# Kernel tuning notes

Measured on AMD Instinct MI355X. Metric: run time of the kernel, lower is better.

The kernel has to match this reference:

```python
import jax, jax.numpy as jnp
import numpy as np

B, LI, LC = 2, 1024, 256
H, NH, HD = 1024, 16, 64
MLP = 4096
EPS = 1e-6


def rmsnorm(x, w):
    return x * jax.lax.rsqrt(jnp.mean(x * x, axis=-1, keepdims=True) + EPS) * w


def apply_rope(x, cos, sin):
    # x: [B, NH, S, HD]; cos/sin: [S, HD]; rotate-half convention
    x1, x2 = jnp.split(x, 2, axis=-1)
    rot = jnp.concatenate([-x2, x1], axis=-1)
    return x * cos + rot * sin


def project_qkv(x, w, b):
    # x: [B, S, H] -> q,k,v each [B, NH, S, HD]
    bsz, s, _ = x.shape
    qkv = (x @ w.T + b).reshape(bsz, s, 3, NH, HD)
    qkv = jnp.transpose(qkv, (2, 0, 3, 1, 4))
    return qkv[0], qkv[1], qkv[2]


def setup_inputs() -> dict:
    key = jax.random.key(0)
    ks = iter(jax.random.split(key, 40))
    n = lambda shape, scale=1.0: jax.random.normal(next(ks), shape, dtype=jnp.float32) * scale
    xav = lambda fo, fi: n((fo, fi), float(np.sqrt(2.0 / (fo + fi))))
    inp = {
        'image_tokens': n((B, LI, H)),
        'condition_tokens': n((B, LC, H)),
        'image_rope_cos': n((LI, HD)),
        'image_rope_sin': n((LI, HD)),
        'cond_rope_cos': n((LC, HD)),
        'cond_rope_sin': n((LC, HD)),
        'img_norm1_w': jnp.ones((H,)), 'cond_norm1_w': jnp.ones((H,)),
        'img_qkv_w': xav(3 * H, H), 'img_qkv_b': jnp.zeros((3 * H,)),
        'cond_qkv_w': xav(3 * H, H), 'cond_qkv_b': jnp.zeros((3 * H,)),
        'img_qn_w': jnp.ones((HD,)), 'img_kn_w': jnp.ones((HD,)),
        'cond_qn_w': jnp.ones((HD,)), 'cond_kn_w': jnp.ones((HD,)),
        'img_out_w': xav(H, H), 'img_out_b': jnp.zeros((H,)),
        'cond_out_w': xav(H, H), 'cond_out_b': jnp.zeros((H,)),
        'img_norm2_w': jnp.ones((H,)), 'cond_norm2_w': jnp.ones((H,)),
        'img_mlp_w1': xav(MLP, H), 'img_mlp_b1': jnp.zeros((MLP,)),
        'img_mlp_w2': xav(MLP, H), 'img_mlp_b2': jnp.zeros((MLP,)),
        'img_mlp_w3': xav(H, MLP), 'img_mlp_b3': jnp.zeros((H,)),
        'cond_mlp_w1': xav(MLP, H), 'cond_mlp_b1': jnp.zeros((MLP,)),
        'cond_mlp_w2': xav(MLP, H), 'cond_mlp_b2': jnp.zeros((MLP,)),
        'cond_mlp_w3': xav(H, MLP), 'cond_mlp_b3': jnp.zeros((H,)),
        'alpha': jnp.zeros((1,)), 'beta': jnp.zeros((1,)),
    }
    return inp


def swiglu(x, w1, b1, w2, b2, w3, b3):
    return (jax.nn.silu(x @ w1.T + b1) * (x @ w2.T + b2)) @ w3.T + b3


def reference(image_tokens, condition_tokens, image_rope_cos, image_rope_sin,
              cond_rope_cos, cond_rope_sin, img_norm1_w, cond_norm1_w,
              img_qkv_w, img_qkv_b, cond_qkv_w, cond_qkv_b,
              img_qn_w, img_kn_w, cond_qn_w, cond_kn_w,
              img_out_w, img_out_b, cond_out_w, cond_out_b,
              img_norm2_w, cond_norm2_w,
              img_mlp_w1, img_mlp_b1, img_mlp_w2, img_mlp_b2, img_mlp_w3, img_mlp_b3,
              cond_mlp_w1, cond_mlp_b1, cond_mlp_w2, cond_mlp_b2, cond_mlp_w3, cond_mlp_b3,
              alpha, beta):
    img_res, cond_res = image_tokens, condition_tokens
    iq, ik, iv = project_qkv(rmsnorm(image_tokens, img_norm1_w), img_qkv_w, img_qkv_b)
    cq, ck, cv = project_qkv(rmsnorm(condition_tokens, cond_norm1_w), cond_qkv_w, cond_qkv_b)
    iq = apply_rope(rmsnorm(iq, img_qn_w), image_rope_cos, image_rope_sin)
    ik = apply_rope(rmsnorm(ik, img_kn_w), image_rope_cos, image_rope_sin)
    cq = apply_rope(rmsnorm(cq, cond_qn_w), cond_rope_cos, cond_rope_sin)
    ck = apply_rope(rmsnorm(ck, cond_kn_w), cond_rope_cos, cond_rope_sin)
    q = jnp.concatenate([cq, iq], axis=2)  # [B, NH, LC+LI, HD]
    k = jnp.concatenate([ck, ik], axis=2)
    v = jnp.concatenate([cv, iv], axis=2)
    scores = jnp.einsum('bhqd,bhkd->bhqk', q, k) / jnp.sqrt(jnp.float32(HD)).astype(q.dtype)
    attn = jax.nn.softmax(scores, axis=-1)
    out = jnp.einsum('bhqk,bhkd->bhqd', attn, v)
    cond_o, img_o = out[:, :, :LC], out[:, :, LC:]
    cond_o = jnp.transpose(cond_o, (0, 2, 1, 3)).reshape(B, LC, H)
    img_o = jnp.transpose(img_o, (0, 2, 1, 3)).reshape(B, LI, H)
    condition_tokens = cond_res + (cond_o @ cond_out_w.T + cond_out_b)
    image_tokens = img_res + alpha.reshape(1, 1, 1) * (img_o @ img_out_w.T + img_out_b)
    condition_tokens = condition_tokens + swiglu(rmsnorm(condition_tokens, cond_norm2_w),
                                                 cond_mlp_w1, cond_mlp_b1, cond_mlp_w2, cond_mlp_b2, cond_mlp_w3, cond_mlp_b3)
    image_tokens = image_tokens + beta.reshape(1, 1, 1) * swiglu(rmsnorm(image_tokens, img_norm2_w),
                                                                 img_mlp_w1, img_mlp_b1, img_mlp_w2, img_mlp_b2, img_mlp_w3, img_mlp_b3)
    return image_tokens, condition_tokens
```

## Files before the change

### kernel.cpp

```cpp
#include <hip/hip_runtime.h>
#include <hip/hip_bf16.h>

#define BB   2
#define LI   1024
#define LC   256
#define SEQ  1280
#define HDIM 1024
#define NH   16
#define HD   64
#define MLPD 4096
#define EPS  1e-6f
#define MROWS 2560
#define MTI  16
#define MTT  20

typedef __bf16 bf16x8 __attribute__((ext_vector_type(8)));
typedef float f32x4 __attribute__((ext_vector_type(4)));
typedef unsigned short us4 __attribute__((ext_vector_type(4)));
typedef unsigned short us8 __attribute__((ext_vector_type(8)));

static __device__ __forceinline__ unsigned short f2bf(float f) {
    unsigned int u = __builtin_bit_cast(unsigned int, f);
    u += 0x7fffu + ((u >> 16) & 1u);
    return (unsigned short)(u >> 16);
}
static __device__ __forceinline__ float bf2f(unsigned short h) {
    unsigned int u = ((unsigned int)h) << 16;
    return __builtin_bit_cast(float, u);
}

static __device__ __forceinline__ void gload_lds16(const void* g, void* l) {
    __builtin_amdgcn_global_load_lds((__attribute__((address_space(1))) void*)(g),
                                     (__attribute__((address_space(3))) void*)(l),
                                     16, 0, 0);
}

__global__ __launch_bounds__(256)
void pack_weights(const float* __restrict__ w1i, const float* __restrict__ w2i,
                  const float* __restrict__ w1c, const float* __restrict__ w2c,
                  const float* __restrict__ w3i, const float* __restrict__ w3c,
                  const float* __restrict__ wqi, const float* __restrict__ wqc,
                  const float* __restrict__ woi, const float* __restrict__ woc,
                  unsigned short* __restrict__ wpi, unsigned short* __restrict__ wpc,
                  unsigned short* __restrict__ w3bi, unsigned short* __restrict__ w3bc,
                  unsigned short* __restrict__ wqbi, unsigned short* __restrict__ wqbc,
                  unsigned short* __restrict__ wobi, unsigned short* __restrict__ wobc)
{
    const int seg = blockIdx.y;
    const float* s0 = nullptr; const float* s1 = nullptr;
    unsigned short* dst = nullptr; int n4 = 0; bool pair = false;
    switch (seg) {
        case 0: pair = true; s0 = w1i; s1 = w2i; dst = wpi;  n4 = 8388608 / 4; break;
        case 1: pair = true; s0 = w1c; s1 = w2c; dst = wpc;  n4 = 8388608 / 4; break;
        case 2: s0 = w3i; dst = w3bi; n4 = 4194304 / 4; break;
        case 3: s0 = w3c; dst = w3bc; n4 = 4194304 / 4; break;
        case 4: s0 = wqi; dst = wqbi; n4 = 3145728 / 4; break;
        case 5: s0 = wqc; dst = wqbc; n4 = 3145728 / 4; break;
        case 6: s0 = woi; dst = wobi; n4 = 1048576 / 4; break;
        case 7: s0 = woc; dst = wobc; n4 = 1048576 / 4; break;
    }
    for (int i = blockIdx.x * 256 + threadIdx.x; i < n4; i += gridDim.x * 256) {
        float4 v;
        if (pair) {
            int p  = i >> 8;
            int k4 = i & 255;
            int g = p >> 4, r = p & 15;
            const float* s = (g & 1) ? s1 : s0;
            v = *(const float4*)&s[((size_t)((g >> 1) * 16 + r)) * 1024 + k4 * 4];
        } else {
            v = ((const float4*)s0)[i];
        }
        us4 o = { f2bf(v.x), f2bf(v.y), f2bf(v.z), f2bf(v.w) };
        ((us4*)dst)[i] = o;
    }
}

__global__ __launch_bounds__(256)
void rmsnorm1(const float* __restrict__ img, const float* __restrict__ cond,
              const float* __restrict__ wi, const float* __restrict__ wc,
              unsigned short* __restrict__ xn)
{
    const int row = blockIdx.x;
    const int t   = threadIdx.x;
    const float* x = (row < 2048) ? img + (size_t)row * HDIM
                                  : cond + (size_t)(row - 2048) * HDIM;
    const float* w = (row < 2048) ? wi : wc;
    float4 v = ((const float4*)x)[t];
    float ss = v.x*v.x + v.y*v.y + v.z*v.z + v.w*v.w;
    for (int o = 32; o > 0; o >>= 1) ss += __shfl_xor(ss, o);
    __shared__ float red[4];
    if ((t & 63) == 0) red[t >> 6] = ss;
    __syncthreads();
    float inv = rsqrtf((red[0]+red[1]+red[2]+red[3]) * (1.0f / HDIM) + EPS);
    float4 wv = ((const float4*)w)[t];
    us4 pk = { f2bf(v.x*inv*wv.x), f2bf(v.y*inv*wv.y),
               f2bf(v.z*inv*wv.z), f2bf(v.w*inv*wv.w) };
    *(us4*)&xn[(size_t)row * HDIM + t * 4] = pk;
}

__global__ __launch_bounds__(256)
void rmsnorm2(const float* __restrict__ img_tok, const float* __restrict__ cond_tok,
              const float* __restrict__ op, const float* __restrict__ wi,
              const float* __restrict__ wc, const float* __restrict__ alpha,
              unsigned short* __restrict__ n2)
{
    const int row = blockIdx.x;
    const int t   = threadIdx.x;
    const bool img = row < 2048;
    const float sc = img ? alpha[0] : 1.0f;
    const float* tok = img ? img_tok + (size_t)row * HDIM
                           : cond_tok + (size_t)(row - 2048) * HDIM;
    const float* w = img ? wi : wc;
    float4 tv = ((const float4*)tok)[t];
    float4 ov = ((const float4*)(op + (size_t)row * HDIM))[t];
    float4 v = { tv.x + sc*ov.x, tv.y + sc*ov.y, tv.z + sc*ov.z, tv.w + sc*ov.w };
    float ss = v.x*v.x + v.y*v.y + v.z*v.z + v.w*v.w;
    for (int o = 32; o > 0; o >>= 1) ss += __shfl_xor(ss, o);
    __shared__ float red[4];
    if ((t & 63) == 0) red[t >> 6] = ss;
    __syncthreads();
    float inv = rsqrtf((red[0]+red[1]+red[2]+red[3]) * (1.0f / HDIM) + EPS);
    float4 wv = ((const float4*)w)[t];
    us4 pk = { f2bf(v.x*inv*wv.x), f2bf(v.y*inv*wv.y),
               f2bf(v.z*inv*wv.z), f2bf(v.w*inv*wv.w) };
    *(us4*)&n2[(size_t)row * HDIM + t * 4] = pk;
}

__global__ __launch_bounds__(256)
void op_init(const float* __restrict__ bi, const float* __restrict__ bc,
             float* __restrict__ op)
{
    const int row = blockIdx.x, t = threadIdx.x;
    const float* b = (row < 2048) ? bi : bc;
    ((float4*)(op + (size_t)row * HDIM))[t] = ((const float4*)b)[t];
}

__global__ __launch_bounds__(256)
void down_init(const float* __restrict__ img_tok, const float* __restrict__ cond_tok,
               const float* __restrict__ op, const float* __restrict__ b3i,
               const float* __restrict__ b3c, const float* __restrict__ alpha,
               const float* __restrict__ beta, float* __restrict__ out)
{
    const int row = blockIdx.x, t = threadIdx.x;
    const bool img = row < 2048;
    const float sa = img ? alpha[0] : 1.0f;
    const float sm = img ? beta[0]  : 1.0f;
    const float* tok = img ? img_tok + (size_t)row * HDIM
                           : cond_tok + (size_t)(row - 2048) * HDIM;
    const float* b3 = img ? b3i : b3c;
    float4 tv = ((const float4*)tok)[t];
    float4 ov = ((const float4*)(op + (size_t)row * HDIM))[t];
    float4 bv = ((const float4*)b3)[t];
    float4 o4 = { tv.x + sa*ov.x + sm*bv.x, tv.y + sa*ov.y + sm*bv.y,
                  tv.z + sa*ov.z + sm*bv.z, tv.w + sa*ov.w + sm*bv.w };
    ((float4*)(out + (size_t)row * HDIM))[t] = o4;
}

__global__ __launch_bounds__(256)
void qkv_gemm(const unsigned short* __restrict__ xn,
              const unsigned short* __restrict__ wqi, const unsigned short* __restrict__ wqc,
              const float* __restrict__ bi, const float* __restrict__ bc,
              unsigned short* __restrict__ qh, unsigned short* __restrict__ kh,
              unsigned short* __restrict__ vt)
{
    __shared__ __align__(16) unsigned short As[128][32];
    __shared__ __align__(16) unsigned short Ws[128][32];

    const int mt = blockIdx.x;
    const bool img = mt < MTI;
    const int row0 = img ? mt * 128 : 2048 + (mt - MTI) * 128;
    const int grow0 = img ? mt * 128 : (mt - MTI) * 128;
    const unsigned short* W = img ? wqi : wqc;
    const float* bias = img ? bi : bc;
    const int bn = blockIdx.y * 128;

    const int t = threadIdx.x, lane = t & 63, wid = t >> 6;
    const int wm = wid >> 1, wn = wid & 1;
    const int srow = (wid << 5) + (lane >> 2);
    const int scol = (lane & 3) << 3;
    const unsigned short* Ag0 = xn + (size_t)(row0 + srow)      * HDIM + scol;
    const unsigned short* Ag1 = xn + (size_t)(row0 + srow + 16) * HDIM + scol;
    const unsigned short* Wg0 = W  + (size_t)(bn + srow)        * HDIM + scol;
    const unsigned short* Wg1 = W  + (size_t)(bn + srow + 16)   * HDIM + scol;
    unsigned short* lA0 = &As[(wid << 5)     ][0];
    unsigned short* lA1 = &As[(wid << 5) + 16][0];
    unsigned short* lW0 = &Ws[(wid << 5)     ][0];
    unsigned short* lW1 = &Ws[(wid << 5) + 16][0];

    const int fr = lane & 15, kg = lane >> 4, ko = kg << 3;
    f32x4 acc[4][4] = {};

    for (int k0 = 0; k0 < HDIM; k0 += 32) {
        __syncthreads();
        gload_lds16(Ag0 + k0, lA0);
        gload_lds16(Ag1 + k0, lA1);
        gload_lds16(Wg0 + k0, lW0);
        gload_lds16(Wg1 + k0, lW1);
        __syncthreads();
        bf16x8 aF[4], bF[4];
#pragma unroll
        for (int m = 0; m < 4; ++m) aF[m] = *(const bf16x8*)&As[wm*64 + m*16 + fr][ko];
#pragma unroll
        for (int n = 0; n < 4; ++n) bF[n] = *(const bf16x8*)&Ws[wn*64 + n*16 + fr][ko];
#pragma unroll
        for (int m = 0; m < 4; ++m)
#pragma unroll
            for (int n = 0; n < 4; ++n)
                acc[m][n] = __builtin_amdgcn_mfma_f32_16x16x32_bf16(aF[m], bF[n], acc[m][n], 0,0,0);
    }

#pragma unroll
    for (int n = 0; n < 4; ++n) {
        const int gc = bn + wn*64 + n*16 + fr;
        const int which = gc >> 10;
        const int h = (gc >> 6) & 15, d = gc & 63;
        const float bv = bias[gc];
#pragma unroll
        for (int m = 0; m < 4; ++m) {
            const int gl0 = grow0 + wm*64 + m*16 + (kg << 2);
            int b, s0;
            if (img) { b = gl0 >> 10; s0 = LC + (gl0 & 1023); }
            else     { b = gl0 >> 8;  s0 = gl0 & 255; }
            if (which == 2) {
                us4 pk = { f2bf(acc[m][n][0] + bv), f2bf(acc[m][n][1] + bv),
                           f2bf(acc[m][n][2] + bv), f2bf(acc[m][n][3] + bv) };
                *(us4*)&vt[(((size_t)(b*NH + h)) * HD + d) * SEQ + s0] = pk;
            } else {
                unsigned short* dst = (which == 0) ? qh : kh;
#pragma unroll
                for (int j = 0; j < 4; ++j)
                    dst[(((size_t)(b*NH + h)) * SEQ + s0 + j) * HD + d] = f2bf(acc[m][n][j] + bv);
            }
        }
    }
}

__global__ __launch_bounds__(256)
void pair_gemm(const unsigned short* __restrict__ n2,
               const unsigned short* __restrict__ wpi, const unsigned short* __restrict__ wpc,
               const float* __restrict__ b1i, const float* __restrict__ b2i,
               const float* __restrict__ b1c, const float* __restrict__ b2c,
               unsigned short* __restrict__ hbf)
{
    __shared__ __align__(16) unsigned short As[128][32];
    __shared__ __align__(16) unsigned short Ws[128][32];

    const int mt = blockIdx.x;
    const bool img = mt < MTI;
    const int row0 = img ? mt * 128 : 2048 + (mt - MTI) * 128;
    const unsigned short* W = img ? wpi : wpc;
    const float* b1 = img ? b1i : b1c;
    const float* b2 = img ? b2i : b2c;
    const int x = blockIdx.y;
    const int bn = x * 128;

    const int t = threadIdx.x, lane = t & 63, wid = t >> 6;
    const int wm = wid >> 1, wn = wid & 1;
    const int srow = (wid << 5) + (lane >> 2);
    const int scol = (lane & 3) << 3;
    const unsigned short* Ag0 = n2 + (size_t)(row0 + srow)      * HDIM + scol;
    const unsigned short* Ag1 = n2 + (size_t)(row0 + srow + 16) * HDIM + scol;
    const unsigned short* Wg0 = W  + (size_t)(bn + srow)        * HDIM + scol;
    const unsigned short* Wg1 = W  + (size_t)(bn + srow + 16)   * HDIM + scol;
    unsigned short* lA0 = &As[(wid << 5)     ][0];
    unsigned short* lA1 = &As[(wid << 5) + 16][0];
    unsigned short* lW0 = &Ws[(wid << 5)     ][0];
    unsigned short* lW1 = &Ws[(wid << 5) + 16][0];

    const int fr = lane & 15, kg = lane >> 4, ko = kg << 3;
    f32x4 acc[4][4] = {};

    for (int k0 = 0; k0 < HDIM; k0 += 32) {
        __syncthreads();
        gload_lds16(Ag0 + k0, lA0);
        gload_lds16(Ag1 + k0, lA1);
        gload_lds16(Wg0 + k0, lW0);
        gload_lds16(Wg1 + k0, lW1);
        __syncthreads();
        bf16x8 aF[4], bF[4];
#pragma unroll
        for (int m = 0; m < 4; ++m) aF[m] = *(const bf16x8*)&As[wm*64 + m*16 + fr][ko];
#pragma unroll
        for (int n = 0; n < 4; ++n) bF[n] = *(const bf16x8*)&Ws[wn*64 + n*16 + fr][ko];
#pragma unroll
        for (int m = 0; m < 4; ++m)
#pragma unroll
            for (int n = 0; n < 4; ++n)
                acc[m][n] = __builtin_amdgcn_mfma_f32_16x16x32_bf16(aF[m], bF[n], acc[m][n], 0,0,0);
    }

#pragma unroll
    for (int p = 0; p < 2; ++p) {
        const int lc = (4*x + 2*wn + p) * 16 + fr;
        const float b1v = b1[lc], b2v = b2[lc];
#pragma unroll
        for (int m = 0; m < 4; ++m) {
#pragma unroll
            for (int j = 0; j < 4; ++j) {
                const int row = row0 + wm*64 + m*16 + (kg << 2) + j;
                float g1 = acc[m][2*p    ][j] + b1v;
                float g2 = acc[m][2*p + 1][j] + b2v;
                float hv = (g1 / (1.0f + __expf(-g1))) * g2;
                hbf[(size_t)row * MLPD + lc] = f2bf(hv);
            }
        }
    }
}

__global__ __launch_bounds__(256)
void skg_gemm(const unsigned short* __restrict__ A, int K,
              const unsigned short* __restrict__ Wimg, const unsigned short* __restrict__ Wcond,
              float* __restrict__ out, int kchunk,
              const float* __restrict__ sci, const float* __restrict__ scc)
{
    __shared__ __align__(16) unsigned short As[128][32];
    __shared__ __align__(16) unsigned short Ws[128][32];

    const int mt = blockIdx.y;
    const bool img = mt < MTI;
    const int row0 = img ? mt * 128 : 2048 + (mt - MTI) * 128;
    const unsigned short* W = img ? Wimg : Wcond;
    const float sc = img ? (sci ? sci[0] : 1.0f) : (scc ? scc[0] : 1.0f);
    const int bn = blockIdx.x * 128;
    const int kbase = blockIdx.z * kchunk;

    const int t = threadIdx.x, lane = t & 63, wid = t >> 6;
    const int wm = wid >> 1, wn = wid & 1;
    const int srow = (wid << 5) + (lane >> 2);
    const int scol = (lane & 3) << 3;
    const unsigned short* Ag0 = A + (size_t)(row0 + srow)      * K + kbase + scol;
    const unsigned short* Ag1 = A + (size_t)(row0 + srow + 16) * K + kbase + scol;
    const unsigned short* Wg0 = W + (size_t)(bn + srow)        * K + kbase + scol;
    const unsigned short* Wg1 = W + (size_t)(bn + srow + 16)   * K + kbase + scol;
    unsigned short* lA0 = &As[(wid << 5)     ][0];
    unsigned short* lA1 = &As[(wid << 5) + 16][0];
    unsigned short* lW0 = &Ws[(wid << 5)     ][0];
    unsigned short* lW1 = &Ws[(wid << 5) + 16][0];

    const int fr = lane & 15, kg = lane >> 4, ko = kg << 3;
    f32x4 acc[4][4] = {};

    for (int k0 = 0; k0 < kchunk; k0 += 32) {
        __syncthreads();
        gload_lds16(Ag0 + k0, lA0);
        gload_lds16(Ag1 + k0, lA1);
        gload_lds16(Wg0 + k0, lW0);
        gload_lds16(Wg1 + k0, lW1);
        __syncthreads();
        bf16x8 aF[4], bF[4];
#pragma unroll
        for (int m = 0; m < 4; ++m) aF[m] = *(const bf16x8*)&As[wm*64 + m*16 + fr][ko];
#pragma unroll
        for (int n = 0; n < 4; ++n) bF[n] = *(const bf16x8*)&Ws[wn*64 + n*16 + fr][ko];
#pragma unroll
        for (int m = 0; m < 4; ++m)
#pragma unroll
            for (int n = 0; n < 4; ++n)
                acc[m][n] = __builtin_amdgcn_mfma_f32_16x16x32_bf16(aF[m], bF[n], acc[m][n], 0,0,0);
    }

#pragma unroll
    for (int n = 0; n < 4; ++n) {
        const int col = bn + wn*64 + n*16 + fr;
#pragma unroll
        for (int m = 0; m < 4; ++m) {
            const int r0 = row0 + wm*64 + m*16 + (kg << 2);
#pragma unroll
            for (int j = 0; j < 4; ++j)
                unsafeAtomicAdd(&out[(size_t)(r0 + j) * HDIM + col], sc * acc[m][n][j]);
        }
    }
}

__launch_bounds__(256)
__global__ void qkv_prep(unsigned short* __restrict__ qh, unsigned short* __restrict__ kh,
                         const float* __restrict__ img_qn, const float* __restrict__ img_kn,
                         const float* __restrict__ cond_qn, const float* __restrict__ cond_kn,
                         const float* __restrict__ icos, const float* __restrict__ isin,
                         const float* __restrict__ ccos, const float* __restrict__ csin)
{
    const int L = blockIdx.x * 4 + (threadIdx.x >> 6);
    const int d = threadIdx.x & 63;
    const int b = L / (NH * SEQ);
    const int rem = L - b * NH * SEQ;
    const int h = rem / SEQ;
    const int s = rem - h * SEQ;

    const float *qw, *kw, *cs, *sn;
    if (s < LC) { qw = cond_qn; kw = cond_kn;
                  cs = ccos + (size_t)s * HD; sn = csin + (size_t)s * HD; }
    else        { qw = img_qn; kw = img_kn;
                  cs = icos + (size_t)(s - LC) * HD; sn = isin + (size_t)(s - LC) * HD; }
    const size_t idx = (((size_t)(b*NH + h)) * SEQ + s) * HD + d;
    float qv = bf2f(qh[idx]);
    float kv = bf2f(kh[idx]);

    float sq = qv * qv;
    for (int o = 32; o > 0; o >>= 1) sq += __shfl_xor(sq, o);
    float qn = qv * rsqrtf(sq * (1.0f / HD) + EPS) * qw[d];
    float sk = kv * kv;
    for (int o = 32; o > 0; o >>= 1) sk += __shfl_xor(sk, o);
    float kn = kv * rsqrtf(sk * (1.0f / HD) + EPS) * kw[d];

    const float c = cs[d], s_ = sn[d];
    float qp = __shfl_xor(qn, 32);
    float kp = __shfl_xor(kn, 32);
    float qrot = (d < 32) ? -qp : qp;
    float krot = (d < 32) ? -kp : kp;
    qh[idx] = f2bf((qn * c + qrot * s_) * 0.125f);
    kh[idx] = f2bf(kn * c + krot * s_);
}

__global__ __launch_bounds__(256)
void attn_mfma(const unsigned short* __restrict__ qg,
               const unsigned short* __restrict__ kg,
               const unsigned short* __restrict__ vtg,
               unsigned short* __restrict__ o)
{
    const int q0  = blockIdx.x * 128;
    const int h   = blockIdx.y;
    const int b   = blockIdx.z;
    const int bh  = b * NH + h;
    const int t   = threadIdx.x;
    const int wid = t >> 6;
    const int lane = t & 63;
    const int g  = lane >> 4;
    const int fr = lane & 15;

    __shared__ __align__(16) unsigned short Ks [2][64 * 64];
    __shared__ __align__(16) unsigned short VTs[2][64 * 64];
    __shared__ __align__(16) unsigned short Ps [4][32][72];

    const unsigned short* qb  = qg  + (size_t)bh * SEQ * HD;
    const unsigned short* kb  = kg  + (size_t)bh * SEQ * HD;
    const unsigned short* vtb = vtg + (size_t)bh * HD * SEQ;

    bf16x8 Qf[2][2];
#pragma unroll
    for (int mt = 0; mt < 2; ++mt)
#pragma unroll
        for (int kc = 0; kc < 2; ++kc)
            Qf[mt][kc] = *(const bf16x8*)&qb[(size_t)(q0 + wid*32 + mt*16 + fr) * HD
                                             + kc*32 + g*8];

    f32x4 O[2][4] = {};
    float mreg[2] = { -3e38f, -3e38f };
    float lreg[2] = { 0.f, 0.f };

#define STAGE(tile_, bufi_)                                                     \
    {                                                                           \
        _Pragma("unroll")                                                       \
        for (int i = 0; i < 2; ++i) {                                           \
            int chbase = i * 256 + wid * 64;                                    \
            int ch = chbase + lane;                                             \
            int r = ch >> 3, c = ch & 7;                                        \
            int cs_ = c ^ (r & 7);                                              \
            gload_lds16(kb  + (size_t)((tile_)*64 + r) * HD + cs_*8,            \
                        &Ks[bufi_][chbase * 8]);                                \
            gload_lds16(vtb + (size_t)r * SEQ + (tile_)*64 + cs_*8,             \
                        &VTs[bufi_][chbase * 8]);                               \
        }                                                                       \
    }

    STAGE(0, 0);
    __syncthreads();
    int buf = 0;

    for (int tile = 0; tile < SEQ / 64; ++tile) {
        if (tile + 1 < SEQ / 64) STAGE(tile + 1, buf ^ 1);

        f32x4 ST[2][4] = {};
#pragma unroll
        for (int kc = 0; kc < 2; ++kc)
#pragma unroll
            for (int nt = 0; nt < 4; ++nt) {
                int r = fr + 16*nt;
                bf16x8 kf = *(const bf16x8*)&Ks[buf][r*64 + (((g + 4*kc) ^ (r & 7)) * 8)];
#pragma unroll
                for (int mt = 0; mt < 2; ++mt)
                    ST[mt][nt] = __builtin_amdgcn_mfma_f32_16x16x32_bf16(
                        kf, Qf[mt][kc], ST[mt][nt], 0, 0, 0);
            }

#pragma unroll
        for (int mt = 0; mt < 2; ++mt) {
            float tm = -3e38f;
#pragma unroll
            for (int nt = 0; nt < 4; ++nt)
#pragma unroll
                for (int j = 0; j < 4; ++j) tm = fmaxf(tm, ST[mt][nt][j]);
            tm = fmaxf(tm, __shfl_xor(tm, 16));
            tm = fmaxf(tm, __shfl_xor(tm, 32));
            float mn = fmaxf(mreg[mt], tm);
            float al = __expf(mreg[mt] - mn);
            mreg[mt] = mn;
            float ls = 0.f;
#pragma unroll
            for (int nt = 0; nt < 4; ++nt) {
#pragma unroll
                for (int j = 0; j < 4; ++j) {
                    float p = __expf(ST[mt][nt][j] - mn);
                    ST[mt][nt][j] = p;
                    ls += p;
                }
            }
            ls += __shfl_xor(ls, 16);
            ls += __shfl_xor(ls, 32);
            lreg[mt] = al * lreg[mt] + ls;
            f32x4 alr;
#pragma unroll
            for (int rg = 0; rg < 4; ++rg) alr[rg] = __shfl(al, 4*g + rg);
#pragma unroll
            for (int dt = 0; dt < 4; ++dt) O[mt][dt] *= alr;
#pragma unroll
            for (int nt = 0; nt < 4; ++nt) {
                us4 pk = { f2bf(ST[mt][nt][0]), f2bf(ST[mt][nt][1]),
                           f2bf(ST[mt][nt][2]), f2bf(ST[mt][nt][3]) };
                *(us4*)&Ps[wid][mt*16 + fr][16*nt + 4*g] = pk;
            }
        }

#pragma unroll
        for (int kc = 0; kc < 2; ++kc) {
            bf16x8 Pf[2];
#pragma unroll
            for (int mt = 0; mt < 2; ++mt)
                Pf[mt] = *(const bf16x8*)&Ps[wid][mt*16 + fr][kc*32 + g*8];
#pragma unroll
            for (int dt = 0; dt < 4; ++dt) {
                int r = fr + 16*dt;
                bf16x8 vf = *(const bf16x8*)&VTs[buf][r*64 + (((g + 4*kc) ^ (r & 7)) * 8)];
#pragma unroll
                for (int mt = 0; mt < 2; ++mt)
                    O[mt][dt] = __builtin_amdgcn_mfma_f32_16x16x32_bf16(
                        Pf[mt], vf, O[mt][dt], 0, 0, 0);
            }
        }

        __syncthreads();
        buf ^= 1;
    }

#pragma unroll
    for (int mt = 0; mt < 2; ++mt) {
        const float linv = 1.0f / lreg[mt];
        f32x4 lv;
#pragma unroll
        for (int rg = 0; rg < 4; ++rg) lv[rg] = __shfl(linv, 4*g + rg);
#pragma unroll
        for (int rg = 0; rg < 4; ++rg) {
            const int s_tok = q0 + wid*32 + mt*16 + 4*g + rg;
            const size_t row = (s_tok < LC) ? (size_t)(2048 + b*LC + s_tok)
                                            : (size_t)(b*LI + (s_tok - LC));
#pragma unroll
            for (int dt = 0; dt < 4; ++dt)
                o[row * HDIM + h*HD + 16*dt + fr] = f2bf(O[mt][dt][rg] * lv[rg]);
        }
    }
#undef STAGE
}

extern "C" void kernel_launch(void* const* d_in, const int* in_sizes, int n_in,
                              void* d_out, int out_size, void* d_ws, size_t ws_size,
                              hipStream_t stream)
{
    const float* image_tokens = (const float*)d_in[0];
    const float* cond_tokens  = (const float*)d_in[1];
    const float* icos  = (const float*)d_in[2];
    const float* isin  = (const float*)d_in[3];
    const float* ccos  = (const float*)d_in[4];
    const float* csin  = (const float*)d_in[5];
    const float* img_n1w  = (const float*)d_in[6];
    const float* cond_n1w = (const float*)d_in[7];
    const float* img_qkv_w  = (const float*)d_in[8];
    const float* img_qkv_b  = (const float*)d_in[9];
    const float* cond_qkv_w = (const float*)d_in[10];
    const float* cond_qkv_b = (const float*)d_in[11];
    const float* img_qn  = (const float*)d_in[12];
    const float* img_kn  = (const float*)d_in[13];
    const float* cond_qn = (const float*)d_in[14];
    const float* cond_kn = (const float*)d_in[15];
    const float* img_out_w  = (const float*)d_in[16];
    const float* img_out_b  = (const float*)d_in[17];
    const float* cond_out_w = (const float*)d_in[18];
    const float* cond_out_b = (const float*)d_in[19];
    const float* img_n2w  = (const float*)d_in[20];
    const float* cond_n2w = (const float*)d_in[21];
    const float* img_w1 = (const float*)d_in[22];
    const float* img_b1 = (const float*)d_in[23];
    const float* img_w2 = (const float*)d_in[24];
    const float* img_b2 = (const float*)d_in[25];
    const float* img_w3 = (const float*)d_in[26];
    const float* img_b3 = (const float*)d_in[27];
    const float* cond_w1 = (const float*)d_in[28];
    const float* cond_b1 = (const float*)d_in[29];
    const float* cond_w2 = (const float*)d_in[30];
    const float* cond_b2 = (const float*)d_in[31];
    const float* cond_w3 = (const float*)d_in[32];
    const float* cond_b3 = (const float*)d_in[33];
    const float* alpha = (const float*)d_in[34];
    const float* beta  = (const float*)d_in[35];

    float* out = (float*)d_out;

    unsigned short* u = (unsigned short*)d_ws;
    unsigned short* wp_i  = u + 0;
    unsigned short* wp_c  = u + 8388608;
    unsigned short* w3b_i = u + 16777216;
    unsigned short* w3b_c = u + 20971520;
    unsigned short* wqb_i = u + 25165824;
    unsigned short* wqb_c = u + 28311552;
    unsigned short* wob_i = u + 31457280;
    unsigned short* wob_c = u + 32505856;
    unsigned short* xn = u + 33554432;
    unsigned short* vt = u + 36175872;
    unsigned short* qh = u + 38797312;
    unsigned short* kh = u + 41418752;
    unsigned short* o  = u + 44040192;
    float*          op = (float*)(u + 38797312);
    unsigned short* n2 = u + 36175872;
    unsigned short* hbf = u + 25165824;

    pack_weights<<<dim3(512, 8), 256, 0, stream>>>(
        img_w1, img_w2, cond_w1, cond_w2, img_w3, cond_w3,
        img_qkv_w, cond_qkv_w, img_out_w, cond_out_w,
        wp_i, wp_c, w3b_i, w3b_c, wqb_i, wqb_c, wob_i, wob_c);

    rmsnorm1<<<MROWS, 256, 0, stream>>>(image_tokens, cond_tokens, img_n1w, cond_n1w, xn);

    qkv_gemm<<<dim3(MTT, 24), 256, 0, stream>>>(
        xn, wqb_i, wqb_c, img_qkv_b, cond_qkv_b, qh, kh, vt);

    qkv_prep<<<BB * NH * SEQ / 4, 256, 0, stream>>>(
        qh, kh, img_qn, img_kn, cond_qn, cond_kn, icos, isin, ccos, csin);

    attn_mfma<<<dim3(SEQ / 128, NH, BB), 256, 0, stream>>>(qh, kh, vt, o);

    op_init<<<MROWS, 256, 0, stream>>>(img_out_b, cond_out_b, op);
    skg_gemm<<<dim3(8, MTT, 2), 256, 0, stream>>>(
        o, HDIM, wob_i, wob_c, op, HDIM / 2, nullptr, nullptr);

    rmsnorm2<<<MROWS, 256, 0, stream>>>(
        image_tokens, cond_tokens, op, img_n2w, cond_n2w, alpha, n2);

    pair_gemm<<<dim3(MTT, 64), 256, 0, stream>>>(
        n2, wp_i, wp_c, img_b1, img_b2, cond_b1, cond_b2, hbf);

    down_init<<<MROWS, 256, 0, stream>>>(
        image_tokens, cond_tokens, op, img_b3, cond_b3, alpha, beta, out);
    skg_gemm<<<dim3(8, MTT, 4), 256, 0, stream>>>(
        hbf, MLPD, w3b_i, w3b_c, out, MLPD / 4, beta, nullptr);
}
```

Measured before the change: 292.8 us.

## Double-buffer LDS in GEMMs and remap blocks for XCD-local cache reuse

Each of the three GEMM kernels now uses two LDS stages: the next K-slice is loaded while MFMAs run on the current one, which drops one barrier per iteration. All GEMM and attention launches become 1D grids whose block index is decoded so that blocks landing on the same XCD (id & 7) share a weight column tile or head. The goal is to hide global-to-LDS latency and raise L2 hit rates on MI355X's per-XCD caches. The cost is twice the LDS per block, which may lower occupancy, and the remapping assumes blocks are dispatched round-robin across eight XCDs.

```diff
diff --git a/kernel.cpp b/kernel.cpp
--- a/kernel.cpp
+++ b/kernel.cpp
@@ -163,16 +163,19 @@
               unsigned short* __restrict__ qh, unsigned short* __restrict__ kh,
               unsigned short* __restrict__ vt)
 {
-    __shared__ __align__(16) unsigned short As[128][32];
-    __shared__ __align__(16) unsigned short Ws[128][32];
-
-    const int mt = blockIdx.x;
+    __shared__ __align__(16) unsigned short As[2][128][32];
+    __shared__ __align__(16) unsigned short Ws[2][128][32];
+
+    const int id  = blockIdx.x;
+    const int xcd = id & 7, idx = id >> 3;
+    const int xcol = xcd * 3 + idx / 20;
+    const int mt   = idx % 20;
     const bool img = mt < MTI;
     const int row0 = img ? mt * 128 : 2048 + (mt - MTI) * 128;
     const int grow0 = img ? mt * 128 : (mt - MTI) * 128;
     const unsigned short* W = img ? wqi : wqc;
     const float* bias = img ? bi : bc;
-    const int bn = blockIdx.y * 128;
+    const int bn = xcol * 128;
 
     const int t = threadIdx.x, lane = t & 63, wid = t >> 6;
     const int wm = wid >> 1, wn = wid & 1;
@@ -182,32 +185,34 @@
     const unsigned short* Ag1 = xn + (size_t)(row0 + srow + 16) * HDIM + scol;
     const unsigned short* Wg0 = W  + (size_t)(bn + srow)        * HDIM + scol;
     const unsigned short* Wg1 = W  + (size_t)(bn + srow + 16)   * HDIM + scol;
-    unsigned short* lA0 = &As[(wid << 5)     ][0];
-    unsigned short* lA1 = &As[(wid << 5) + 16][0];
-    unsigned short* lW0 = &Ws[(wid << 5)     ][0];
-    unsigned short* lW1 = &Ws[(wid << 5) + 16][0];
 
     const int fr = lane & 15, kg = lane >> 4, ko = kg << 3;
     f32x4 acc[4][4] = {};
 
-    for (int k0 = 0; k0 < HDIM; k0 += 32) {
-        __syncthreads();
-        gload_lds16(Ag0 + k0, lA0);
-        gload_lds16(Ag1 + k0, lA1);
-        gload_lds16(Wg0 + k0, lW0);
-        gload_lds16(Wg1 + k0, lW1);
-        __syncthreads();
+#define STAGE_Q(k0_, b_) {                                        \
+        gload_lds16(Ag0 + (k0_), &As[b_][(wid << 5)     ][0]);    \
+        gload_lds16(Ag1 + (k0_), &As[b_][(wid << 5) + 16][0]);    \
+        gload_lds16(Wg0 + (k0_), &Ws[b_][(wid << 5)     ][0]);    \
+        gload_lds16(Wg1 + (k0_), &Ws[b_][(wid << 5) + 16][0]); }
+
+    STAGE_Q(0, 0);
+    __syncthreads();
+    for (int k0 = 0, kk = 0; k0 < HDIM; k0 += 32, ++kk) {
+        const int cur = kk & 1;
+        if (k0 + 32 < HDIM) STAGE_Q(k0 + 32, cur ^ 1);
         bf16x8 aF[4], bF[4];
 #pragma unroll
-        for (int m = 0; m < 4; ++m) aF[m] = *(const bf16x8*)&As[wm*64 + m*16 + fr][ko];
-#pragma unroll
-        for (int n = 0; n < 4; ++n) bF[n] = *(const bf16x8*)&Ws[wn*64 + n*16 + fr][ko];
+        for (int m = 0; m < 4; ++m) aF[m] = *(const bf16x8*)&As[cur][wm*64 + m*16 + fr][ko];
+#pragma unroll
+        for (int n = 0; n < 4; ++n) bF[n] = *(const bf16x8*)&Ws[cur][wn*64 + n*16 + fr][ko];
 #pragma unroll
         for (int m = 0; m < 4; ++m)
 #pragma unroll
             for (int n = 0; n < 4; ++n)
                 acc[m][n] = __builtin_amdgcn_mfma_f32_16x16x32_bf16(aF[m], bF[n], acc[m][n], 0,0,0);
-    }
+        __syncthreads();
+    }
+#undef STAGE_Q
 
 #pragma unroll
     for (int n = 0; n < 4; ++n) {
@@ -242,16 +247,18 @@
                const float* __restrict__ b1c, const float* __restrict__ b2c,
                unsigned short* __restrict__ hbf)
 {
-    __shared__ __align__(16) unsigned short As[128][32];
-    __shared__ __align__(16) unsigned short Ws[128][32];
-
-    const int mt = blockIdx.x;
+    __shared__ __align__(16) unsigned short As[2][128][32];
+    __shared__ __align__(16) unsigned short Ws[2][128][32];
+
+    const int id  = blockIdx.x;
+    const int xcd = id & 7, idx = id >> 3;
+    const int x   = xcd * 8 + idx / 20;
+    const int mt  = idx % 20;
     const bool img = mt < MTI;
     const int row0 = img ? mt * 128 : 2048 + (mt - MTI) * 128;
     const unsigned short* W = img ? wpi : wpc;
     const float* b1 = img ? b1i : b1c;
     const float* b2 = img ? b2i : b2c;
-    const int x = blockIdx.y;
     const int bn = x * 128;
 
     const int t = threadIdx.x, lane = t & 63, wid = t >> 6;
@@ -262,32 +269,34 @@
     const unsigned short* Ag1 = n2 + (size_t)(row0 + srow + 16) * HDIM + scol;
     const unsigned short* Wg0 = W  + (size_t)(bn + srow)        * HDIM + scol;
     const unsigned short* Wg1 = W  + (size_t)(bn + srow + 16)   * HDIM + scol;
-    unsigned short* lA0 = &As[(wid << 5)     ][0];
-    unsigned short* lA1 = &As[(wid << 5) + 16][0];
-    unsigned short* lW0 = &Ws[(wid << 5)     ][0];
-    unsigned short* lW1 = &Ws[(wid << 5) + 16][0];
 
     const int fr = lane & 15, kg = lane >> 4, ko = kg << 3;
     f32x4 acc[4][4] = {};
 
-    for (int k0 = 0; k0 < HDIM; k0 += 32) {
-        __syncthreads();
-        gload_lds16(Ag0 + k0, lA0);
-        gload_lds16(Ag1 + k0, lA1);
-        gload_lds16(Wg0 + k0, lW0);
-        gload_lds16(Wg1 + k0, lW1);
-        __syncthreads();
+#define STAGE_P(k0_, b_) {                                        \
+        gload_lds16(Ag0 + (k0_), &As[b_][(wid << 5)     ][0]);    \
+        gload_lds16(Ag1 + (k0_), &As[b_][(wid << 5) + 16][0]);    \
+        gload_lds16(Wg0 + (k0_), &Ws[b_][(wid << 5)     ][0]);    \
+        gload_lds16(Wg1 + (k0_), &Ws[b_][(wid << 5) + 16][0]); }
+
+    STAGE_P(0, 0);
+    __syncthreads();
+    for (int k0 = 0, kk = 0; k0 < HDIM; k0 += 32, ++kk) {
+        const int cur = kk & 1;
+        if (k0 + 32 < HDIM) STAGE_P(k0 + 32, cur ^ 1);
         bf16x8 aF[4], bF[4];
 #pragma unroll
-        for (int m = 0; m < 4; ++m) aF[m] = *(const bf16x8*)&As[wm*64 + m*16 + fr][ko];
-#pragma unroll
-        for (int n = 0; n < 4; ++n) bF[n] = *(const bf16x8*)&Ws[wn*64 + n*16 + fr][ko];
+        for (int m = 0; m < 4; ++m) aF[m] = *(const bf16x8*)&As[cur][wm*64 + m*16 + fr][ko];
+#pragma unroll
+        for (int n = 0; n < 4; ++n) bF[n] = *(const bf16x8*)&Ws[cur][wn*64 + n*16 + fr][ko];
 #pragma unroll
         for (int m = 0; m < 4; ++m)
 #pragma unroll
             for (int n = 0; n < 4; ++n)
                 acc[m][n] = __builtin_amdgcn_mfma_f32_16x16x32_bf16(aF[m], bF[n], acc[m][n], 0,0,0);
-    }
+        __syncthreads();
+    }
+#undef STAGE_P
 
 #pragma unroll
     for (int p = 0; p < 2; ++p) {
@@ -313,16 +322,19 @@
               float* __restrict__ out, int kchunk,
               const float* __restrict__ sci, const float* __restrict__ scc)
 {
-    __shared__ __align__(16) unsigned short As[128][32];
-    __shared__ __align__(16) unsigned short Ws[128][32];
-
-    const int mt = blockIdx.y;
+    __shared__ __align__(16) unsigned short As[2][128][32];
+    __shared__ __align__(16) unsigned short Ws[2][128][32];
+
+    const int id  = blockIdx.x;
+    const int xcd = id & 7, idx = id >> 3;
+    const int bn  = xcd * 128;
+    const int mt  = idx % 20;
+    const int kz  = idx / 20;
     const bool img = mt < MTI;
     const int row0 = img ? mt * 128 : 2048 + (mt - MTI) * 128;
     const unsigned short* W = img ? Wimg : Wcond;
     const float sc = img ? (sci ? sci[0] : 1.0f) : (scc ? scc[0] : 1.0f);
-    const int bn = blockIdx.x * 128;
-    const int kbase = blockIdx.z * kchunk;
+    const int kbase = kz * kchunk;
 
     const int t = threadIdx.x, lane = t & 63, wid = t >> 6;
     const int wm = wid >> 1, wn = wid & 1;
@@ -332,32 +344,34 @@
     const unsigned short* Ag1 = A + (size_t)(row0 + srow + 16) * K + kbase + scol;
     const unsigned short* Wg0 = W + (size_t)(bn + srow)        * K + kbase + scol;
     const unsigned short* Wg1 = W + (size_t)(bn + srow + 16)   * K + kbase + scol;
-    unsigned short* lA0 = &As[(wid << 5)     ][0];
-    unsigned short* lA1 = &As[(wid << 5) + 16][0];
-    unsigned short* lW0 = &Ws[(wid << 5)     ][0];
-    unsigned short* lW1 = &Ws[(wid << 5) + 16][0];
 
     const int fr = lane & 15, kg = lane >> 4, ko = kg << 3;
     f32x4 acc[4][4] = {};
 
-    for (int k0 = 0; k0 < kchunk; k0 += 32) {
-        __syncthreads();
-        gload_lds16(Ag0 + k0, lA0);
-        gload_lds16(Ag1 + k0, lA1);
-        gload_lds16(Wg0 + k0, lW0);
-        gload_lds16(Wg1 + k0, lW1);
-        __syncthreads();
+#define STAGE_S(k0_, b_) {                                        \
+        gload_lds16(Ag0 + (k0_), &As[b_][(wid << 5)     ][0]);    \
+        gload_lds16(Ag1 + (k0_), &As[b_][(wid << 5) + 16][0]);    \
+        gload_lds16(Wg0 + (k0_), &Ws[b_][(wid << 5)     ][0]);    \
+        gload_lds16(Wg1 + (k0_), &Ws[b_][(wid << 5) + 16][0]); }
+
+    STAGE_S(0, 0);
+    __syncthreads();
+    for (int k0 = 0, kk = 0; k0 < kchunk; k0 += 32, ++kk) {
+        const int cur = kk & 1;
+        if (k0 + 32 < kchunk) STAGE_S(k0 + 32, cur ^ 1);
         bf16x8 aF[4], bF[4];
 #pragma unroll
-        for (int m = 0; m < 4; ++m) aF[m] = *(const bf16x8*)&As[wm*64 + m*16 + fr][ko];
-#pragma unroll
-        for (int n = 0; n < 4; ++n) bF[n] = *(const bf16x8*)&Ws[wn*64 + n*16 + fr][ko];
+        for (int m = 0; m < 4; ++m) aF[m] = *(const bf16x8*)&As[cur][wm*64 + m*16 + fr][ko];
+#pragma unroll
+        for (int n = 0; n < 4; ++n) bF[n] = *(const bf16x8*)&Ws[cur][wn*64 + n*16 + fr][ko];
 #pragma unroll
         for (int m = 0; m < 4; ++m)
 #pragma unroll
             for (int n = 0; n < 4; ++n)
                 acc[m][n] = __builtin_amdgcn_mfma_f32_16x16x32_bf16(aF[m], bF[n], acc[m][n], 0,0,0);
-    }
+        __syncthreads();
+    }
+#undef STAGE_S
 
 #pragma unroll
     for (int n = 0; n < 4; ++n) {
@@ -417,10 +431,12 @@
                const unsigned short* __restrict__ vtg,
                unsigned short* __restrict__ o)
 {
-    const int q0  = blockIdx.x * 128;
-    const int h   = blockIdx.y;
-    const int b   = blockIdx.z;
-    const int bh  = b * NH + h;
+    const int id  = blockIdx.x;
+    const int xcd = id & 7, idx = id >> 3;
+    const int bh  = xcd * 4 + idx / 10;
+    const int q0  = (idx % 10) * 128;
+    const int h   = bh & 15;
+    const int b   = bh >> 4;
     const int t   = threadIdx.x;
     const int wid = t >> 6;
     const int lane = t & 63;
@@ -628,26 +644,26 @@
 
     rmsnorm1<<<MROWS, 256, 0, stream>>>(image_tokens, cond_tokens, img_n1w, cond_n1w, xn);
 
-    qkv_gemm<<<dim3(MTT, 24), 256, 0, stream>>>(
+    qkv_gemm<<<480, 256, 0, stream>>>(
         xn, wqb_i, wqb_c, img_qkv_b, cond_qkv_b, qh, kh, vt);
 
     qkv_prep<<<BB * NH * SEQ / 4, 256, 0, stream>>>(
         qh, kh, img_qn, img_kn, cond_qn, cond_kn, icos, isin, ccos, csin);
 
-    attn_mfma<<<dim3(SEQ / 128, NH, BB), 256, 0, stream>>>(qh, kh, vt, o);
+    attn_mfma<<<320, 256, 0, stream>>>(qh, kh, vt, o);
 
     op_init<<<MROWS, 256, 0, stream>>>(img_out_b, cond_out_b, op);
-    skg_gemm<<<dim3(8, MTT, 2), 256, 0, stream>>>(
+    skg_gemm<<<8 * MTT * 2, 256, 0, stream>>>(
         o, HDIM, wob_i, wob_c, op, HDIM / 2, nullptr, nullptr);
 
     rmsnorm2<<<MROWS, 256, 0, stream>>>(
         image_tokens, cond_tokens, op, img_n2w, cond_n2w, alpha, n2);
 
-    pair_gemm<<<dim3(MTT, 64), 256, 0, stream>>>(
+    pair_gemm<<<1280, 256, 0, stream>>>(
         n2, wp_i, wp_c, img_b1, img_b2, cond_b1, cond_b2, hbf);
 
     down_init<<<MROWS, 256, 0, stream>>>(
         image_tokens, cond_tokens, op, img_b3, cond_b3, alpha, beta, out);
-    skg_gemm<<<dim3(8, MTT, 4), 256, 0, stream>>>(
+    skg_gemm<<<8 * MTT * 4, 256, 0, stream>>>(
         hbf, MLPD, w3b_i, w3b_c, out, MLPD / 4, beta, nullptr);
 }
```

Result: no change. 298.4 us (+1.9%).

## Remap GEMM and attention grids to XCD-aware 1D order; widen pair_gemm K tile with swizzle

Applied to the files above, without the earlier changes.

Flattens the launch grids of qkv_gemm, attn_mfma, skg_gemm and pair_gemm to 1D and decodes the block id so that blocks landing on the same XCD (round-robin id&7) share the same weight column tile or the same batch-head. The goal is better L2 reuse of the weight and K/V tiles within each XCD. Separately, pair_gemm moves to a 64-wide K tile with an XOR-swizzled LDS layout, which halves the number of barrier pairs and avoids LDS bank conflicts. The cost is more index arithmetic per block, and the mapping relies on grid sizes that divide exactly.

```diff
diff --git a/kernel.cpp b/kernel.cpp
--- a/kernel.cpp
+++ b/kernel.cpp
@@ -166,13 +166,16 @@
     __shared__ __align__(16) unsigned short As[128][32];
     __shared__ __align__(16) unsigned short Ws[128][32];
 
-    const int mt = blockIdx.x;
+    const int id  = blockIdx.x;
+    const int xcd = id & 7, idx = id >> 3;
+    const int xcol = xcd * 3 + idx / 20;
+    const int mt   = idx % 20;
     const bool img = mt < MTI;
     const int row0 = img ? mt * 128 : 2048 + (mt - MTI) * 128;
     const int grow0 = img ? mt * 128 : (mt - MTI) * 128;
     const unsigned short* W = img ? wqi : wqc;
     const float* bias = img ? bi : bc;
-    const int bn = blockIdx.y * 128;
+    const int bn = xcol * 128;
 
     const int t = threadIdx.x, lane = t & 63, wid = t >> 6;
     const int wm = wid >> 1, wn = wid & 1;
@@ -242,51 +245,62 @@
                const float* __restrict__ b1c, const float* __restrict__ b2c,
                unsigned short* __restrict__ hbf)
 {
-    __shared__ __align__(16) unsigned short As[128][32];
-    __shared__ __align__(16) unsigned short Ws[128][32];
-
-    const int mt = blockIdx.x;
+    __shared__ __align__(16) unsigned short As[128][64];
+    __shared__ __align__(16) unsigned short Ws[128][64];
+
+    const int id  = blockIdx.x;
+    const int xcd = id & 7, idx = id >> 3;
+    const int x   = xcd * 8 + idx / 20;
+    const int mt  = idx % 20;
     const bool img = mt < MTI;
     const int row0 = img ? mt * 128 : 2048 + (mt - MTI) * 128;
     const unsigned short* W = img ? wpi : wpc;
     const float* b1 = img ? b1i : b1c;
     const float* b2 = img ? b2i : b2c;
-    const int x = blockIdx.y;
     const int bn = x * 128;
 
     const int t = threadIdx.x, lane = t & 63, wid = t >> 6;
     const int wm = wid >> 1, wn = wid & 1;
-    const int srow = (wid << 5) + (lane >> 2);
-    const int scol = (lane & 3) << 3;
-    const unsigned short* Ag0 = n2 + (size_t)(row0 + srow)      * HDIM + scol;
-    const unsigned short* Ag1 = n2 + (size_t)(row0 + srow + 16) * HDIM + scol;
-    const unsigned short* Wg0 = W  + (size_t)(bn + srow)        * HDIM + scol;
-    const unsigned short* Wg1 = W  + (size_t)(bn + srow + 16)   * HDIM + scol;
-    unsigned short* lA0 = &As[(wid << 5)     ][0];
-    unsigned short* lA1 = &As[(wid << 5) + 16][0];
-    unsigned short* lW0 = &Ws[(wid << 5)     ][0];
-    unsigned short* lW1 = &Ws[(wid << 5) + 16][0];
-
-    const int fr = lane & 15, kg = lane >> 4, ko = kg << 3;
+    const int fr = lane & 15, kg = lane >> 4;
+
+    const int ch_r[4] = { ((wid*4+0)*64 + lane) >> 3, ((wid*4+1)*64 + lane) >> 3,
+                          ((wid*4+2)*64 + lane) >> 3, ((wid*4+3)*64 + lane) >> 3 };
+    const int ch_c[4] = { (((wid*4+0)*64 + lane) & 7) ^ (ch_r[0] & 7),
+                          (((wid*4+1)*64 + lane) & 7) ^ (ch_r[1] & 7),
+                          (((wid*4+2)*64 + lane) & 7) ^ (ch_r[2] & 7),
+                          (((wid*4+3)*64 + lane) & 7) ^ (ch_r[3] & 7) };
+
     f32x4 acc[4][4] = {};
 
-    for (int k0 = 0; k0 < HDIM; k0 += 32) {
+    for (int k0 = 0; k0 < HDIM; k0 += 64) {
         __syncthreads();
-        gload_lds16(Ag0 + k0, lA0);
-        gload_lds16(Ag1 + k0, lA1);
-        gload_lds16(Wg0 + k0, lW0);
-        gload_lds16(Wg1 + k0, lW1);
+#pragma unroll
+        for (int i = 0; i < 4; ++i) {
+            gload_lds16(n2 + (size_t)(row0 + ch_r[i]) * HDIM + k0 + ch_c[i]*8,
+                        &As[0][0] + (size_t)(wid*4 + i) * 64 * 8);
+            gload_lds16(W  + (size_t)(bn   + ch_r[i]) * HDIM + k0 + ch_c[i]*8,
+                        &Ws[0][0] + (size_t)(wid*4 + i) * 64 * 8);
+        }
         __syncthreads();
-        bf16x8 aF[4], bF[4];
-#pragma unroll
-        for (int m = 0; m < 4; ++m) aF[m] = *(const bf16x8*)&As[wm*64 + m*16 + fr][ko];
-#pragma unroll
-        for (int n = 0; n < 4; ++n) bF[n] = *(const bf16x8*)&Ws[wn*64 + n*16 + fr][ko];
-#pragma unroll
-        for (int m = 0; m < 4; ++m)
-#pragma unroll
-            for (int n = 0; n < 4; ++n)
-                acc[m][n] = __builtin_amdgcn_mfma_f32_16x16x32_bf16(aF[m], bF[n], acc[m][n], 0,0,0);
+#pragma unroll
+        for (int kc = 0; kc < 2; ++kc) {
+            bf16x8 aF[4], bF[4];
+#pragma unroll
+            for (int m = 0; m < 4; ++m) {
+                const int r = wm*64 + m*16 + fr;
+                aF[m] = *(const bf16x8*)&As[r][(((kc*4 + kg) ^ (r & 7)) << 3)];
+            }
+#pragma unroll
+            for (int n = 0; n < 4; ++n) {
+                const int r = wn*64 + n*16 + fr;
+                bF[n] = *(const bf16x8*)&Ws[r][(((kc*4 + kg) ^ (r & 7)) << 3)];
+            }
+#pragma unroll
+            for (int m = 0; m < 4; ++m)
+#pragma unroll
+                for (int n = 0; n < 4; ++n)
+                    acc[m][n] = __builtin_amdgcn_mfma_f32_16x16x32_bf16(aF[m], bF[n], acc[m][n], 0,0,0);
+        }
     }
 
 #pragma unroll
@@ -316,13 +330,16 @@
     __shared__ __align__(16) unsigned short As[128][32];
     __shared__ __align__(16) unsigned short Ws[128][32];
 
-    const int mt = blockIdx.y;
+    const int id  = blockIdx.x;
+    const int xcd = id & 7, idx = id >> 3;
+    const int bn  = xcd * 128;
+    const int mt  = idx % 20;
+    const int kz  = idx / 20;
     const bool img = mt < MTI;
     const int row0 = img ? mt * 128 : 2048 + (mt - MTI) * 128;
     const unsigned short* W = img ? Wimg : Wcond;
     const float sc = img ? (sci ? sci[0] : 1.0f) : (scc ? scc[0] : 1.0f);
-    const int bn = blockIdx.x * 128;
-    const int kbase = blockIdx.z * kchunk;
+    const int kbase = kz * kchunk;
 
     const int t = threadIdx.x, lane = t & 63, wid = t >> 6;
     const int wm = wid >> 1, wn = wid & 1;
@@ -417,10 +434,12 @@
                const unsigned short* __restrict__ vtg,
                unsigned short* __restrict__ o)
 {
-    const int q0  = blockIdx.x * 128;
-    const int h   = blockIdx.y;
-    const int b   = blockIdx.z;
-    const int bh  = b * NH + h;
+    const int id  = blockIdx.x;
+    const int xcd = id & 7, idx = id >> 3;
+    const int bh  = xcd * 4 + idx / 10;
+    const int q0  = (idx % 10) * 128;
+    const int h   = bh & 15;
+    const int b   = bh >> 4;
     const int t   = threadIdx.x;
     const int wid = t >> 6;
     const int lane = t & 63;
@@ -628,26 +647,26 @@
 
     rmsnorm1<<<MROWS, 256, 0, stream>>>(image_tokens, cond_tokens, img_n1w, cond_n1w, xn);
 
-    qkv_gemm<<<dim3(MTT, 24), 256, 0, stream>>>(
+    qkv_gemm<<<480, 256, 0, stream>>>(
         xn, wqb_i, wqb_c, img_qkv_b, cond_qkv_b, qh, kh, vt);
 
     qkv_prep<<<BB * NH * SEQ / 4, 256, 0, stream>>>(
         qh, kh, img_qn, img_kn, cond_qn, cond_kn, icos, isin, ccos, csin);
 
-    attn_mfma<<<dim3(SEQ / 128, NH, BB), 256, 0, stream>>>(qh, kh, vt, o);
+    attn_mfma<<<320, 256, 0, stream>>>(qh, kh, vt, o);
 
     op_init<<<MROWS, 256, 0, stream>>>(img_out_b, cond_out_b, op);
-    skg_gemm<<<dim3(8, MTT, 2), 256, 0, stream>>>(
+    skg_gemm<<<8 * MTT * 2, 256, 0, stream>>>(
         o, HDIM, wob_i, wob_c, op, HDIM / 2, nullptr, nullptr);
 
     rmsnorm2<<<MROWS, 256, 0, stream>>>(
         image_tokens, cond_tokens, op, img_n2w, cond_n2w, alpha, n2);
 
-    pair_gemm<<<dim3(MTT, 64), 256, 0, stream>>>(
+    pair_gemm<<<1280, 256, 0, stream>>>(
         n2, wp_i, wp_c, img_b1, img_b2, cond_b1, cond_b2, hbf);
 
     down_init<<<MROWS, 256, 0, stream>>>(
         image_tokens, cond_tokens, op, img_b3, cond_b3, alpha, beta, out);
-    skg_gemm<<<dim3(8, MTT, 4), 256, 0, stream>>>(
+    skg_gemm<<<8 * MTT * 4, 256, 0, stream>>>(
         hbf, MLPD, w3b_i, w3b_c, out, MLPD / 4, beta, nullptr);
 }
```

Result: no change. 296.2 us (+1.2%).
